# Performance work log

Hardware: AMD Instinct MI355X
Metric: run time of the kernel (lower is better)

## Reference

```python
import jax, jax.numpy as jnp
import numpy as np

D_MODEL = 1024
N_HEADS = 16
D_HEAD = D_MODEL // N_HEADS
SCALE = 1.0 / np.sqrt(D_HEAD)


def setup_inputs() -> dict:
    key = jax.random.key(0)
    ks = jax.random.split(key, 5)
    B, S = 2, 2048
    x = jax.random.normal(ks[0], (B, S, D_MODEL), dtype=jnp.float32)
    # torch F.linear weights have shape (d_out, d_in); kaiming-uniform-ish init
    bound = 1.0 / np.sqrt(D_MODEL)
    Wq = jax.random.uniform(ks[1], (D_MODEL, D_MODEL), jnp.float32, -bound, bound)
    Wk = jax.random.uniform(ks[2], (D_MODEL, D_MODEL), jnp.float32, -bound, bound)
    Wv = jax.random.uniform(ks[3], (D_MODEL, D_MODEL), jnp.float32, -bound, bound)
    Wo = jax.random.uniform(ks[4], (D_MODEL, D_MODEL), jnp.float32, -bound, bound)
    return {"x": x, "Wq": Wq, "Wk": Wk, "Wv": Wv, "Wo": Wo}


def reference(x, Wq, Wk, Wv, Wo):
    B, S, _ = x.shape
    # F.linear(x, W) = x @ W.T; reshape to [B, H, S, Dh]
    def proj(W):
        return (x @ W.T).reshape(B, S, N_HEADS, D_HEAD).transpose(0, 2, 1, 3)
    Q, K, V = proj(Wq), proj(Wk), proj(Wv)
    # scores [B, H, S, S]
    attn = jnp.einsum('bhqd,bhkd->bhqk', Q, K) * SCALE
    causal = jnp.tril(jnp.ones((S, S), dtype=bool))
    attn = jnp.where(causal, attn, -jnp.inf)
    attn = jax.nn.softmax(attn, axis=-1)
    out = jnp.einsum('bhqk,bhkd->bhqd', attn, V)
    out = out.transpose(0, 2, 1, 3).reshape(B, S, D_MODEL)
    return out @ Wo.T
```

## Files before the change

### kernel.cpp

```cpp
#include <hip/hip_runtime.h>


typedef __attribute__((ext_vector_type(8))) short short8;
typedef __attribute__((ext_vector_type(4))) float f32x4;
typedef __attribute__((ext_vector_type(4))) _Float16 half4;

#if __has_builtin(__builtin_amdgcn_exp2f)
#define EXP2F(x) __builtin_amdgcn_exp2f(x)
#else
#define EXP2F(x) exp2f(x)
#endif

__device__ __forceinline__ unsigned short f2bf(float f) {
  unsigned int x = __float_as_uint(f);
  x += 0x7fffu + ((x >> 16) & 1u);
  return (unsigned short)(x >> 16);
}

__device__ __forceinline__ void gload16(const void* g, void* l) {
  __builtin_amdgcn_global_load_lds(
      (const __attribute__((address_space(1))) void*)g,
      (__attribute__((address_space(3))) void*)l, 16, 0, 0);
}

__device__ __forceinline__ int swz64(int row, int sc) {
  return row * 64 + ((((sc >> 3) ^ (row & 7)) << 3) | (sc & 7));
}

__global__ void cast5_kernel(const float* __restrict__ x, const float* __restrict__ wq,
                             const float* __restrict__ wk, const float* __restrict__ wv,
                             const float* __restrict__ wo,
                             unsigned short* __restrict__ xb, unsigned short* __restrict__ wqb,
                             unsigned short* __restrict__ wkb, unsigned short* __restrict__ wvb,
                             unsigned short* __restrict__ wob) {
  const float* in; unsigned short* out; int n4; float sc = 1.f;
  switch (blockIdx.y) {
    case 0: in = x;  out = xb;  n4 = 1048576; break;
    case 1: in = wq; out = wqb; n4 = 262144; sc = 0.18033688011112042f; break;
    case 2: in = wk; out = wkb; n4 = 262144; break;
    case 3: in = wv; out = wvb; n4 = 262144; break;
    default: in = wo; out = wob; n4 = 262144; break;
  }
  int i = blockIdx.x * 256 + threadIdx.x;
  if (i >= n4) return;
  float4 v = ((const float4*)in)[i];
  union { unsigned short u[4]; uint2 p; } o;
  o.u[0] = f2bf(v.x * sc); o.u[1] = f2bf(v.y * sc);
  o.u[2] = f2bf(v.z * sc); o.u[3] = f2bf(v.w * sc);
  ((uint2*)out)[i] = o.p;
}

#define GK 1024

__global__ __launch_bounds__(256) void gemm_qkv_kernel(
    const unsigned short* __restrict__ X,
    const unsigned short* __restrict__ Wq,
    const unsigned short* __restrict__ Wk,
    const unsigned short* __restrict__ Wv,
    unsigned short* __restrict__ Qo,
    unsigned short* __restrict__ Ko,
    _Float16* __restrict__ Vt) {
  __shared__ unsigned short As[128 * 32];
  __shared__ unsigned short Bs[128 * 32];
  int mb = blockIdx.x;
  int nbT = blockIdx.y;
  int sel = nbT >> 3, nb = nbT & 7;
  const unsigned short* W = sel == 0 ? Wq : (sel == 1 ? Wk : Wv);

  int tid = threadIdx.x;
  int w = tid >> 6, l = tid & 63, quad = l >> 4, lo = l & 15;
  int wm = (w >> 1) * 64, wn = (w & 1) * 64;

  f32x4 acc[4][4];
#pragma unroll
  for (int i = 0; i < 4; i++)
#pragma unroll
    for (int j = 0; j < 4; j++) acc[i][j] = (f32x4){0.f, 0.f, 0.f, 0.f};

  for (int k0 = 0; k0 < GK; k0 += 32) {
    __syncthreads();
#pragma unroll
    for (int i = 0; i < 2; i++) {
      int c = i * 256 + tid;
      gload16(X + (size_t)(mb * 128 + (c >> 2)) * GK + k0 + (c & 3) * 8,
              (char*)As + c * 16);
      gload16(W + (size_t)(nb * 128 + (c >> 2)) * GK + k0 + (c & 3) * 8,
              (char*)Bs + c * 16);
    }
    __syncthreads();
    short8 a[4], b[4];
#pragma unroll
    for (int mi = 0; mi < 4; mi++)
      a[mi] = *(const short8*)&As[(wm + mi * 16 + lo) * 32 + quad * 8];
#pragma unroll
    for (int ni = 0; ni < 4; ni++)
      b[ni] = *(const short8*)&Bs[(wn + ni * 16 + lo) * 32 + quad * 8];
#pragma unroll
    for (int mi = 0; mi < 4; mi++)
#pragma unroll
      for (int ni = 0; ni < 4; ni++)
        acc[mi][ni] = __builtin_amdgcn_mfma_f32_16x16x32_bf16(a[mi], b[ni],
                                                              acc[mi][ni], 0, 0, 0);
  }
  if (sel == 2) {
#pragma unroll
    for (int mi = 0; mi < 4; mi++)
#pragma unroll
      for (int ni = 0; ni < 4; ni++) {
        int row0 = mb * 128 + wm + mi * 16 + quad * 4;
        int col = nb * 128 + wn + ni * 16 + lo;
        int bb = row0 >> 11, ss = row0 & 2047;
        int hh = col >> 6, dd = col & 63;
        half4 v;
#pragma unroll
        for (int r = 0; r < 4; r++) v[r] = (_Float16)acc[mi][ni][r];
        *(half4*)&Vt[((size_t)((bb * 16 + hh) * 64 + dd)) * 2048 + ss] = v;
      }
  } else {
    unsigned short* C = sel == 0 ? Qo : Ko;
#pragma unroll
    for (int mi = 0; mi < 4; mi++)
#pragma unroll
      for (int ni = 0; ni < 4; ni++)
#pragma unroll
        for (int r = 0; r < 4; r++) {
          int row = mb * 128 + wm + mi * 16 + quad * 4 + r;
          int col = nb * 128 + wn + ni * 16 + lo;
          C[(size_t)row * 1024 + col] = f2bf(acc[mi][ni][r]);
        }
  }
}

__global__ __launch_bounds__(256) void gemm_out_kernel(
    const unsigned short* __restrict__ A,
    const unsigned short* __restrict__ W,
    float* __restrict__ C) {
  __shared__ unsigned short As[128 * 32];
  __shared__ unsigned short Bs[64 * 32];
  int mb = blockIdx.x, nb = blockIdx.y;
  int tid = threadIdx.x;
  int w = tid >> 6, l = tid & 63, quad = l >> 4, lo = l & 15;
  int wm = w * 32;

  f32x4 acc[2][4];
#pragma unroll
  for (int i = 0; i < 2; i++)
#pragma unroll
    for (int j = 0; j < 4; j++) acc[i][j] = (f32x4){0.f, 0.f, 0.f, 0.f};

  for (int k0 = 0; k0 < GK; k0 += 32) {
    __syncthreads();
#pragma unroll
    for (int i = 0; i < 2; i++) {
      int c = i * 256 + tid;
      gload16(A + (size_t)(mb * 128 + (c >> 2)) * GK + k0 + (c & 3) * 8,
              (char*)As + c * 16);
    }
    gload16(W + (size_t)(nb * 64 + (tid >> 2)) * GK + k0 + (tid & 3) * 8,
            (char*)Bs + tid * 16);
    __syncthreads();
    short8 a[2], b[4];
#pragma unroll
    for (int mi = 0; mi < 2; mi++)
      a[mi] = *(const short8*)&As[(wm + mi * 16 + lo) * 32 + quad * 8];
#pragma unroll
    for (int ni = 0; ni < 4; ni++)
      b[ni] = *(const short8*)&Bs[(ni * 16 + lo) * 32 + quad * 8];
#pragma unroll
    for (int mi = 0; mi < 2; mi++)
#pragma unroll
      for (int ni = 0; ni < 4; ni++)
        acc[mi][ni] = __builtin_amdgcn_mfma_f32_16x16x32_bf16(a[mi], b[ni],
                                                              acc[mi][ni], 0, 0, 0);
  }
#pragma unroll
  for (int mi = 0; mi < 2; mi++)
#pragma unroll
    for (int ni = 0; ni < 4; ni++)
#pragma unroll
      for (int r = 0; r < 4; r++) {
        int row = mb * 128 + wm + mi * 16 + quad * 4 + r;
        int col = nb * 64 + ni * 16 + lo;
        C[(size_t)row * 1024 + col] = acc[mi][ni][r];
      }
}

__global__ __launch_bounds__(256) void attn_kernel(
    const unsigned short* __restrict__ Q,
    const unsigned short* __restrict__ K,
    const _Float16* __restrict__ Vt,
    unsigned short* __restrict__ O) {
  const int S = 2048, DM = 1024;
  __shared__ unsigned short Qs[64 * 64];
  __shared__ unsigned short Ks[2][64 * 64];
  __shared__ _Float16 Vts[2][64 * 64];

  int id = blockIdx.x;
  int bh = id & 31;
  int qt = 31 - (id >> 5);
  int b = bh >> 4, h = bh & 15;
  size_t base = (size_t)b * S * DM + h * 64;
  size_t baseVt = (size_t)(bh * 64) * S;

  int tid = threadIdx.x;
  int w = tid >> 6, lane = tid & 63, quad = lane >> 4, lo = lane & 15;
  int qrow0 = qt * 64 + w * 16;

#pragma unroll
  for (int j = 0; j < 2; j++) {
    int s_ = j * 256 + tid;
    int row = s_ >> 3, lc = (s_ & 7) ^ (row & 7);
    gload16(Q + base + (size_t)(qt * 64 + row) * DM + lc * 8, (char*)Qs + s_ * 16);
  }
#pragma unroll
  for (int j = 0; j < 2; j++) {
    int s_ = j * 256 + tid;
    int row = s_ >> 3, lc = (s_ & 7) ^ (row & 7);
    gload16(K + base + (size_t)row * DM + lc * 8, (char*)Ks[0] + s_ * 16);
    gload16(Vt + baseVt + (size_t)row * S + lc * 8, (char*)Vts[0] + s_ * 16);
  }

  short8 qf[2];
  f32x4 oacc[4];
  float m_ = -1e30f, l_ = 0.f;
#pragma unroll
  for (int ni = 0; ni < 4; ni++) oacc[ni] = (f32x4){0.f, 0.f, 0.f, 0.f};

  int tend = qt + 1;
  for (int t = 0; t < tend; t++) {
    __syncthreads();
    if (t + 1 < tend) {
      int tb = (t + 1) & 1;
#pragma unroll
      for (int j = 0; j < 2; j++) {
        int s_ = j * 256 + tid;
        int row = s_ >> 3, lc = (s_ & 7) ^ (row & 7);
        gload16(K + base + (size_t)((t + 1) * 64 + row) * DM + lc * 8,
                (char*)Ks[tb] + s_ * 16);
        gload16(Vt + baseVt + (size_t)row * S + (t + 1) * 64 + lc * 8,
                (char*)Vts[tb] + s_ * 16);
      }
    }
    if (t == 0) {
#pragma unroll
      for (int d = 0; d < 2; d++)
        qf[d] = *(const short8*)&Qs[swz64(w * 16 + lo, d * 32 + quad * 8)];
    }
    const unsigned short* ks = Ks[t & 1];
    const _Float16* vs = Vts[t & 1];

    f32x4 st[4];
#pragma unroll
    for (int kvt = 0; kvt < 4; kvt++) st[kvt] = (f32x4){0.f, 0.f, 0.f, 0.f};
#pragma unroll
    for (int kvt = 0; kvt < 4; kvt++)
#pragma unroll
      for (int d = 0; d < 2; d++) {
        short8 kf = *(const short8*)&ks[swz64(kvt * 16 + lo, d * 32 + quad * 8)];
        st[kvt] = __builtin_amdgcn_mfma_f32_16x16x32_bf16(kf, qf[d], st[kvt], 0, 0, 0);
      }

    float z[4][4];
#pragma unroll
    for (int kvt = 0; kvt < 4; kvt++)
#pragma unroll
      for (int r = 0; r < 4; r++) z[kvt][r] = st[kvt][r];
    if (t == tend - 1) {
      int qg = qrow0 + lo;
#pragma unroll
      for (int kvt = 0; kvt < 4; kvt++)
#pragma unroll
        for (int r = 0; r < 4; r++) {
          int kv = t * 64 + kvt * 16 + quad * 4 + r;
          if (kv > qg) z[kvt][r] = -1e30f;
        }
    }

    float mx = z[0][0];
#pragma unroll
    for (int kvt = 0; kvt < 4; kvt++)
#pragma unroll
      for (int r = 0; r < 4; r++) mx = fmaxf(mx, z[kvt][r]);
    mx = fmaxf(mx, __shfl_xor(mx, 16));
    mx = fmaxf(mx, __shfl_xor(mx, 32));
    float mnew = fmaxf(m_, mx);
    float alpha = EXP2F(m_ - mnew);
    m_ = mnew;
    float rs = 0.f;
    half4 pf[4];
#pragma unroll
    for (int kvt = 0; kvt < 4; kvt++) {
      half4 p4;
#pragma unroll
      for (int r = 0; r < 4; r++) {
        float p = EXP2F(z[kvt][r] - mnew);
        p4[r] = (_Float16)p;
        rs += p;
      }
      pf[kvt] = p4;
    }
    rs += __shfl_xor(rs, 16);
    rs += __shfl_xor(rs, 32);
    l_ = l_ * alpha + rs;
    float ab[4];
#pragma unroll
    for (int r = 0; r < 4; r++) ab[r] = __shfl(alpha, (lane & 48) + quad * 4 + r);
#pragma unroll
    for (int ni = 0; ni < 4; ni++)
#pragma unroll
      for (int r = 0; r < 4; r++) oacc[ni][r] *= ab[r];

#pragma unroll
    for (int kvt = 0; kvt < 4; kvt++)
#pragma unroll
      for (int ni = 0; ni < 4; ni++) {
        half4 vf = *(const half4*)&vs[swz64(ni * 16 + lo, kvt * 16 + quad * 4)];
        oacc[ni] = __builtin_amdgcn_mfma_f32_16x16x16f16(pf[kvt], vf, oacc[ni], 0, 0, 0);
      }
  }

  float inv[4];
#pragma unroll
  for (int r = 0; r < 4; r++)
    inv[r] = 1.0f / __shfl(l_, (lane & 48) + quad * 4 + r);
#pragma unroll
  for (int ni = 0; ni < 4; ni++)
#pragma unroll
    for (int r = 0; r < 4; r++) {
      int qg = qrow0 + quad * 4 + r;
      O[base + (size_t)qg * DM + ni * 16 + lo] = f2bf(oacc[ni][r] * inv[r]);
    }
}

extern "C" void kernel_launch(void* const* d_in, const int* in_sizes, int n_in,
                              void* d_out, int out_size, void* d_ws, size_t ws_size,
                              hipStream_t stream) {
  const float* x  = (const float*)d_in[0];
  const float* Wq = (const float*)d_in[1];
  const float* Wk = (const float*)d_in[2];
  const float* Wv = (const float*)d_in[3];
  const float* Wo = (const float*)d_in[4];
  float* out = (float*)d_out;
  char* ws = (char*)d_ws;

  unsigned short* Xb  = (unsigned short*)(ws);
  unsigned short* Wqb = (unsigned short*)(ws + (8ll  << 20));
  unsigned short* Wkb = (unsigned short*)(ws + (10ll << 20));
  unsigned short* Wvb = (unsigned short*)(ws + (12ll << 20));
  unsigned short* Wob = (unsigned short*)(ws + (14ll << 20));
  unsigned short* Qb  = (unsigned short*)(ws + (16ll << 20));
  unsigned short* Kb  = (unsigned short*)(ws + (24ll << 20));
  _Float16*       Vt  = (_Float16*)     (ws + (32ll << 20));
  unsigned short* Ob  = (unsigned short*)(ws + (40ll << 20));

  cast5_kernel<<<dim3(4096, 5), 256, 0, stream>>>(x, Wq, Wk, Wv, Wo,
                                                  Xb, Wqb, Wkb, Wvb, Wob);
  gemm_qkv_kernel<<<dim3(32, 24), 256, 0, stream>>>(Xb, Wqb, Wkb, Wvb, Qb, Kb, Vt);
  attn_kernel<<<1024, 256, 0, stream>>>(Qb, Kb, Vt, Ob);
  gemm_out_kernel<<<dim3(32, 16), 256, 0, stream>>>(Ob, Wob, out);
}
```

Before: 193.2 us.

## Double-buffer GEMM loads, pair causal attention tiles, compact cast grid

Both GEMM kernels now use two LDS buffers and prefetch the next K-slice while computing the current one, removing one barrier per iteration. The attention kernel launches half as many blocks, and each block processes a short and a long causal query tile to balance work across blocks. The softmax row sum is now accumulated with an MFMA against a ones vector instead of shuffles. The cast kernel uses a flat grid so no idle blocks are launched for the smaller weight matrices. Attention gets fewer, longer blocks, which may reduce overlap between blocks, and the GEMMs use more LDS per block.

```diff
diff --git a/kernel.cpp b/kernel.cpp
--- a/kernel.cpp
+++ b/kernel.cpp
@@ -27,22 +27,26 @@
   return row * 64 + ((((sc >> 3) ^ (row & 7)) << 3) | (sc & 7));
 }
 
-__global__ void cast5_kernel(const float* __restrict__ x, const float* __restrict__ wq,
-                             const float* __restrict__ wk, const float* __restrict__ wv,
-                             const float* __restrict__ wo,
-                             unsigned short* __restrict__ xb, unsigned short* __restrict__ wqb,
-                             unsigned short* __restrict__ wkb, unsigned short* __restrict__ wvb,
-                             unsigned short* __restrict__ wob) {
-  const float* in; unsigned short* out; int n4; float sc = 1.f;
-  switch (blockIdx.y) {
-    case 0: in = x;  out = xb;  n4 = 1048576; break;
-    case 1: in = wq; out = wqb; n4 = 262144; sc = 0.18033688011112042f; break;
-    case 2: in = wk; out = wkb; n4 = 262144; break;
-    case 3: in = wv; out = wvb; n4 = 262144; break;
-    default: in = wo; out = wob; n4 = 262144; break;
-  }
-  int i = blockIdx.x * 256 + threadIdx.x;
-  if (i >= n4) return;
+__global__ void cast_kernel(const float* __restrict__ x, const float* __restrict__ wq,
+                            const float* __restrict__ wk, const float* __restrict__ wv,
+                            const float* __restrict__ wo,
+                            unsigned short* __restrict__ xb, unsigned short* __restrict__ wqb,
+                            unsigned short* __restrict__ wkb, unsigned short* __restrict__ wvb,
+                            unsigned short* __restrict__ wob) {
+  int id = blockIdx.x;
+  const float* in; unsigned short* out; int blk; float sc = 1.f;
+  if (id < 4096) { in = x; out = xb; blk = id; }
+  else {
+    int wsel = (id - 4096) >> 10;
+    blk = (id - 4096) & 1023;
+    switch (wsel) {
+      case 0: in = wq; out = wqb; sc = 0.18033688011112042f; break;
+      case 1: in = wk; out = wkb; break;
+      case 2: in = wv; out = wvb; break;
+      default: in = wo; out = wob; break;
+    }
+  }
+  int i = blk * 256 + threadIdx.x;
   float4 v = ((const float4*)in)[i];
   union { unsigned short u[4]; uint2 p; } o;
   o.u[0] = f2bf(v.x * sc); o.u[1] = f2bf(v.y * sc);
@@ -60,8 +64,8 @@
     unsigned short* __restrict__ Qo,
     unsigned short* __restrict__ Ko,
     _Float16* __restrict__ Vt) {
-  __shared__ unsigned short As[128 * 32];
-  __shared__ unsigned short Bs[128 * 32];
+  __shared__ unsigned short As[2][128 * 32];
+  __shared__ unsigned short Bs[2][128 * 32];
   int mb = blockIdx.x;
   int nbT = blockIdx.y;
   int sel = nbT >> 3, nb = nbT & 7;
@@ -77,24 +81,35 @@
 #pragma unroll
     for (int j = 0; j < 4; j++) acc[i][j] = (f32x4){0.f, 0.f, 0.f, 0.f};
 
-  for (int k0 = 0; k0 < GK; k0 += 32) {
+#pragma unroll
+  for (int i = 0; i < 2; i++) {
+    int c = i * 256 + tid;
+    gload16(X + (size_t)(mb * 128 + (c >> 2)) * GK + (c & 3) * 8, (char*)As[0] + c * 16);
+    gload16(W + (size_t)(nb * 128 + (c >> 2)) * GK + (c & 3) * 8, (char*)Bs[0] + c * 16);
+  }
+
+  for (int kt = 0; kt < 32; kt++) {
     __syncthreads();
-#pragma unroll
-    for (int i = 0; i < 2; i++) {
-      int c = i * 256 + tid;
-      gload16(X + (size_t)(mb * 128 + (c >> 2)) * GK + k0 + (c & 3) * 8,
-              (char*)As + c * 16);
-      gload16(W + (size_t)(nb * 128 + (c >> 2)) * GK + k0 + (c & 3) * 8,
-              (char*)Bs + c * 16);
-    }
-    __syncthreads();
+    if (kt + 1 < 32) {
+      int nb_ = (kt + 1) & 1, k0 = (kt + 1) * 32;
+#pragma unroll
+      for (int i = 0; i < 2; i++) {
+        int c = i * 256 + tid;
+        gload16(X + (size_t)(mb * 128 + (c >> 2)) * GK + k0 + (c & 3) * 8,
+                (char*)As[nb_] + c * 16);
+        gload16(W + (size_t)(nb * 128 + (c >> 2)) * GK + k0 + (c & 3) * 8,
+                (char*)Bs[nb_] + c * 16);
+      }
+    }
+    const unsigned short* as = As[kt & 1];
+    const unsigned short* bs = Bs[kt & 1];
     short8 a[4], b[4];
 #pragma unroll
     for (int mi = 0; mi < 4; mi++)
-      a[mi] = *(const short8*)&As[(wm + mi * 16 + lo) * 32 + quad * 8];
+      a[mi] = *(const short8*)&as[(wm + mi * 16 + lo) * 32 + quad * 8];
 #pragma unroll
     for (int ni = 0; ni < 4; ni++)
-      b[ni] = *(const short8*)&Bs[(wn + ni * 16 + lo) * 32 + quad * 8];
+      b[ni] = *(const short8*)&bs[(wn + ni * 16 + lo) * 32 + quad * 8];
 #pragma unroll
     for (int mi = 0; mi < 4; mi++)
 #pragma unroll
@@ -135,8 +150,8 @@
     const unsigned short* __restrict__ A,
     const unsigned short* __restrict__ W,
     float* __restrict__ C) {
-  __shared__ unsigned short As[128 * 32];
-  __shared__ unsigned short Bs[64 * 32];
+  __shared__ unsigned short As[2][128 * 32];
+  __shared__ unsigned short Bs[2][64 * 32];
   int mb = blockIdx.x, nb = blockIdx.y;
   int tid = threadIdx.x;
   int w = tid >> 6, l = tid & 63, quad = l >> 4, lo = l & 15;
@@ -148,24 +163,35 @@
 #pragma unroll
     for (int j = 0; j < 4; j++) acc[i][j] = (f32x4){0.f, 0.f, 0.f, 0.f};
 
-  for (int k0 = 0; k0 < GK; k0 += 32) {
+#pragma unroll
+  for (int i = 0; i < 2; i++) {
+    int c = i * 256 + tid;
+    gload16(A + (size_t)(mb * 128 + (c >> 2)) * GK + (c & 3) * 8, (char*)As[0] + c * 16);
+  }
+  gload16(W + (size_t)(nb * 64 + (tid >> 2)) * GK + (tid & 3) * 8, (char*)Bs[0] + tid * 16);
+
+  for (int kt = 0; kt < 32; kt++) {
     __syncthreads();
-#pragma unroll
-    for (int i = 0; i < 2; i++) {
-      int c = i * 256 + tid;
-      gload16(A + (size_t)(mb * 128 + (c >> 2)) * GK + k0 + (c & 3) * 8,
-              (char*)As + c * 16);
-    }
-    gload16(W + (size_t)(nb * 64 + (tid >> 2)) * GK + k0 + (tid & 3) * 8,
-            (char*)Bs + tid * 16);
-    __syncthreads();
+    if (kt + 1 < 32) {
+      int nb_ = (kt + 1) & 1, k0 = (kt + 1) * 32;
+#pragma unroll
+      for (int i = 0; i < 2; i++) {
+        int c = i * 256 + tid;
+        gload16(A + (size_t)(mb * 128 + (c >> 2)) * GK + k0 + (c & 3) * 8,
+                (char*)As[nb_] + c * 16);
+      }
+      gload16(W + (size_t)(nb * 64 + (tid >> 2)) * GK + k0 + (tid & 3) * 8,
+              (char*)Bs[nb_] + tid * 16);
+    }
+    const unsigned short* as = As[kt & 1];
+    const unsigned short* bs = Bs[kt & 1];
     short8 a[2], b[4];
 #pragma unroll
     for (int mi = 0; mi < 2; mi++)
-      a[mi] = *(const short8*)&As[(wm + mi * 16 + lo) * 32 + quad * 8];
+      a[mi] = *(const short8*)&as[(wm + mi * 16 + lo) * 32 + quad * 8];
 #pragma unroll
     for (int ni = 0; ni < 4; ni++)
-      b[ni] = *(const short8*)&Bs[(ni * 16 + lo) * 32 + quad * 8];
+      b[ni] = *(const short8*)&bs[(ni * 16 + lo) * 32 + quad * 8];
 #pragma unroll
     for (int mi = 0; mi < 2; mi++)
 #pragma unroll
@@ -197,139 +223,131 @@
 
   int id = blockIdx.x;
   int bh = id & 31;
-  int qt = 31 - (id >> 5);
+  int lsel = id >> 5;
   int b = bh >> 4, h = bh & 15;
   size_t base = (size_t)b * S * DM + h * 64;
   size_t baseVt = (size_t)(bh * 64) * S;
 
   int tid = threadIdx.x;
   int w = tid >> 6, lane = tid & 63, quad = lane >> 4, lo = lane & 15;
-  int qrow0 = qt * 64 + w * 16;
-
-#pragma unroll
-  for (int j = 0; j < 2; j++) {
-    int s_ = j * 256 + tid;
-    int row = s_ >> 3, lc = (s_ & 7) ^ (row & 7);
-    gload16(Q + base + (size_t)(qt * 64 + row) * DM + lc * 8, (char*)Qs + s_ * 16);
-  }
-#pragma unroll
-  for (int j = 0; j < 2; j++) {
-    int s_ = j * 256 + tid;
-    int row = s_ >> 3, lc = (s_ & 7) ^ (row & 7);
-    gload16(K + base + (size_t)row * DM + lc * 8, (char*)Ks[0] + s_ * 16);
-    gload16(Vt + baseVt + (size_t)row * S + lc * 8, (char*)Vts[0] + s_ * 16);
-  }
-
-  short8 qf[2];
-  f32x4 oacc[4];
-  float m_ = -1e30f, l_ = 0.f;
-#pragma unroll
-  for (int ni = 0; ni < 4; ni++) oacc[ni] = (f32x4){0.f, 0.f, 0.f, 0.f};
-
-  int tend = qt + 1;
-  for (int t = 0; t < tend; t++) {
+  const half4 ones = {(_Float16)1.f, (_Float16)1.f, (_Float16)1.f, (_Float16)1.f};
+
+  for (int phase = 0; phase < 2; phase++) {
+    int qt = phase ? (31 - lsel) : lsel;
+    int qrow0 = qt * 64 + w * 16;
     __syncthreads();
-    if (t + 1 < tend) {
-      int tb = (t + 1) & 1;
-#pragma unroll
-      for (int j = 0; j < 2; j++) {
-        int s_ = j * 256 + tid;
-        int row = s_ >> 3, lc = (s_ & 7) ^ (row & 7);
-        gload16(K + base + (size_t)((t + 1) * 64 + row) * DM + lc * 8,
-                (char*)Ks[tb] + s_ * 16);
-        gload16(Vt + baseVt + (size_t)row * S + (t + 1) * 64 + lc * 8,
-                (char*)Vts[tb] + s_ * 16);
-      }
-    }
-    if (t == 0) {
-#pragma unroll
-      for (int d = 0; d < 2; d++)
-        qf[d] = *(const short8*)&Qs[swz64(w * 16 + lo, d * 32 + quad * 8)];
-    }
-    const unsigned short* ks = Ks[t & 1];
-    const _Float16* vs = Vts[t & 1];
-
-    f32x4 st[4];
-#pragma unroll
-    for (int kvt = 0; kvt < 4; kvt++) st[kvt] = (f32x4){0.f, 0.f, 0.f, 0.f};
-#pragma unroll
-    for (int kvt = 0; kvt < 4; kvt++)
-#pragma unroll
-      for (int d = 0; d < 2; d++) {
-        short8 kf = *(const short8*)&ks[swz64(kvt * 16 + lo, d * 32 + quad * 8)];
-        st[kvt] = __builtin_amdgcn_mfma_f32_16x16x32_bf16(kf, qf[d], st[kvt], 0, 0, 0);
-      }
-
-    float z[4][4];
-#pragma unroll
-    for (int kvt = 0; kvt < 4; kvt++)
-#pragma unroll
-      for (int r = 0; r < 4; r++) z[kvt][r] = st[kvt][r];
-    if (t == tend - 1) {
-      int qg = qrow0 + lo;
+
+#pragma unroll
+    for (int j = 0; j < 2; j++) {
+      int s_ = j * 256 + tid;
+      int row = s_ >> 3, lc = (s_ & 7) ^ (row & 7);
+      gload16(Q + base + (size_t)(qt * 64 + row) * DM + lc * 8, (char*)Qs + s_ * 16);
+      gload16(K + base + (size_t)row * DM + lc * 8, (char*)Ks[0] + s_ * 16);
+      gload16(Vt + baseVt + (size_t)row * S + lc * 8, (char*)Vts[0] + s_ * 16);
+    }
+
+    short8 qf[2];
+    f32x4 oacc[4], lacc;
+    float m_ = -1e30f;
+    lacc = (f32x4){0.f, 0.f, 0.f, 0.f};
+#pragma unroll
+    for (int ni = 0; ni < 4; ni++) oacc[ni] = (f32x4){0.f, 0.f, 0.f, 0.f};
+
+    int tend = qt + 1;
+    for (int t = 0; t < tend; t++) {
+      __syncthreads();
+      if (t + 1 < tend) {
+        int tb = (t + 1) & 1;
+#pragma unroll
+        for (int j = 0; j < 2; j++) {
+          int s_ = j * 256 + tid;
+          int row = s_ >> 3, lc = (s_ & 7) ^ (row & 7);
+          gload16(K + base + (size_t)((t + 1) * 64 + row) * DM + lc * 8,
+                  (char*)Ks[tb] + s_ * 16);
+          gload16(Vt + baseVt + (size_t)row * S + (t + 1) * 64 + lc * 8,
+                  (char*)Vts[tb] + s_ * 16);
+        }
+      }
+      if (t == 0) {
+#pragma unroll
+        for (int d = 0; d < 2; d++)
+          qf[d] = *(const short8*)&Qs[swz64(w * 16 + lo, d * 32 + quad * 8)];
+      }
+      const unsigned short* ks = Ks[t & 1];
+      const _Float16* vs = Vts[t & 1];
+
+      f32x4 st[4];
+#pragma unroll
+      for (int kvt = 0; kvt < 4; kvt++) st[kvt] = (f32x4){0.f, 0.f, 0.f, 0.f};
 #pragma unroll
       for (int kvt = 0; kvt < 4; kvt++)
 #pragma unroll
-        for (int r = 0; r < 4; r++) {
-          int kv = t * 64 + kvt * 16 + quad * 4 + r;
-          if (kv > qg) z[kvt][r] = -1e30f;
+        for (int d = 0; d < 2; d++) {
+          short8 kf = *(const short8*)&ks[swz64(kvt * 16 + lo, d * 32 + quad * 8)];
+          st[kvt] = __builtin_amdgcn_mfma_f32_16x16x32_bf16(kf, qf[d], st[kvt], 0, 0, 0);
         }
-    }
-
-    float mx = z[0][0];
-#pragma unroll
-    for (int kvt = 0; kvt < 4; kvt++)
-#pragma unroll
-      for (int r = 0; r < 4; r++) mx = fmaxf(mx, z[kvt][r]);
-    mx = fmaxf(mx, __shfl_xor(mx, 16));
-    mx = fmaxf(mx, __shfl_xor(mx, 32));
-    float mnew = fmaxf(m_, mx);
-    float alpha = EXP2F(m_ - mnew);
-    m_ = mnew;
-    float rs = 0.f;
-    half4 pf[4];
-#pragma unroll
-    for (int kvt = 0; kvt < 4; kvt++) {
-      half4 p4;
+
+      if (t == tend - 1) {
+        int qg = qrow0 + lo;
+#pragma unroll
+        for (int kvt = 0; kvt < 4; kvt++)
+#pragma unroll
+          for (int r = 0; r < 4; r++) {
+            int kv = t * 64 + kvt * 16 + quad * 4 + r;
+            if (kv > qg) st[kvt][r] = -1e30f;
+          }
+      }
+
+      float mx = st[0][0];
+#pragma unroll
+      for (int kvt = 0; kvt < 4; kvt++)
+#pragma unroll
+        for (int r = 0; r < 4; r++) mx = fmaxf(mx, st[kvt][r]);
+      mx = fmaxf(mx, __shfl_xor(mx, 16));
+      mx = fmaxf(mx, __shfl_xor(mx, 32));
+      float mnew = fmaxf(m_, mx);
+      float alpha = EXP2F(m_ - mnew);
+      m_ = mnew;
+      half4 pf[4];
+#pragma unroll
+      for (int kvt = 0; kvt < 4; kvt++) {
+        half4 p4;
+#pragma unroll
+        for (int r = 0; r < 4; r++) p4[r] = (_Float16)EXP2F(st[kvt][r] - mnew);
+        pf[kvt] = p4;
+      }
+      float ab[4];
+#pragma unroll
+      for (int r = 0; r < 4; r++) ab[r] = __shfl(alpha, (lane & 48) + quad * 4 + r);
+#pragma unroll
+      for (int ni = 0; ni < 4; ni++)
+#pragma unroll
+        for (int r = 0; r < 4; r++) oacc[ni][r] *= ab[r];
+#pragma unroll
+      for (int r = 0; r < 4; r++) lacc[r] *= ab[r];
+
+#pragma unroll
+      for (int kvt = 0; kvt < 4; kvt++) {
+#pragma unroll
+        for (int ni = 0; ni < 4; ni++) {
+          half4 vf = *(const half4*)&vs[swz64(ni * 16 + lo, kvt * 16 + quad * 4)];
+          oacc[ni] = __builtin_amdgcn_mfma_f32_16x16x16f16(pf[kvt], vf, oacc[ni], 0, 0, 0);
+        }
+        lacc = __builtin_amdgcn_mfma_f32_16x16x16f16(pf[kvt], ones, lacc, 0, 0, 0);
+      }
+    }
+
+    float inv[4];
+#pragma unroll
+    for (int r = 0; r < 4; r++) inv[r] = 1.0f / lacc[r];
+#pragma unroll
+    for (int ni = 0; ni < 4; ni++)
 #pragma unroll
       for (int r = 0; r < 4; r++) {
-        float p = EXP2F(z[kvt][r] - mnew);
-        p4[r] = (_Float16)p;
-        rs += p;
-      }
-      pf[kvt] = p4;
-    }
-    rs += __shfl_xor(rs, 16);
-    rs += __shfl_xor(rs, 32);
-    l_ = l_ * alpha + rs;
-    float ab[4];
-#pragma unroll
-    for (int r = 0; r < 4; r++) ab[r] = __shfl(alpha, (lane & 48) + quad * 4 + r);
-#pragma unroll
-    for (int ni = 0; ni < 4; ni++)
-#pragma unroll
-      for (int r = 0; r < 4; r++) oacc[ni][r] *= ab[r];
-
-#pragma unroll
-    for (int kvt = 0; kvt < 4; kvt++)
-#pragma unroll
-      for (int ni = 0; ni < 4; ni++) {
-        half4 vf = *(const half4*)&vs[swz64(ni * 16 + lo, kvt * 16 + quad * 4)];
-        oacc[ni] = __builtin_amdgcn_mfma_f32_16x16x16f16(pf[kvt], vf, oacc[ni], 0, 0, 0);
-      }
-  }
-
-  float inv[4];
-#pragma unroll
-  for (int r = 0; r < 4; r++)
-    inv[r] = 1.0f / __shfl(l_, (lane & 48) + quad * 4 + r);
-#pragma unroll
-  for (int ni = 0; ni < 4; ni++)
-#pragma unroll
-    for (int r = 0; r < 4; r++) {
-      int qg = qrow0 + quad * 4 + r;
-      O[base + (size_t)qg * DM + ni * 16 + lo] = f2bf(oacc[ni][r] * inv[r]);
-    }
+        int qg = qrow0 + quad * 4 + r;
+        O[base + (size_t)qg * DM + ni * 16 + lo] = f2bf(oacc[ni][r] * inv[r]);
+      }
+  }
 }
 
 extern "C" void kernel_launch(void* const* d_in, const int* in_sizes, int n_in,
@@ -353,9 +371,8 @@
   _Float16*       Vt  = (_Float16*)     (ws + (32ll << 20));
   unsigned short* Ob  = (unsigned short*)(ws + (40ll << 20));
 
-  cast5_kernel<<<dim3(4096, 5), 256, 0, stream>>>(x, Wq, Wk, Wv, Wo,
-                                                  Xb, Wqb, Wkb, Wvb, Wob);
+  cast_kernel<<<8192, 256, 0, stream>>>(x, Wq, Wk, Wv, Wo, Xb, Wqb, Wkb, Wvb, Wob);
   gemm_qkv_kernel<<<dim3(32, 24), 256, 0, stream>>>(Xb, Wqb, Wkb, Wvb, Qb, Kb, Vt);
-  attn_kernel<<<1024, 256, 0, stream>>>(Qb, Kb, Vt, Ob);
+  attn_kernel<<<512, 256, 0, stream>>>(Qb, Kb, Vt, Ob);
   gemm_out_kernel<<<dim3(32, 16), 256, 0, stream>>>(Ob, Wob, out);
 }
```

New measurement: 187.7 us. 2.9% less time.
